# Kernel tuning notes

Hardware: AMD Instinct MI355X
Metric: run time of the kernel (lower is better)

Reference implementation:

```python
import jax, jax.numpy as jnp
import numpy as np

N = 8192        # num nodes (bs in the original docstring)
D_IN = 512      # input feature dim
HEADS = 8
DPH = 512 // HEADS  # size_per_head = hidden_size // num_heads
EDGE_P = 0.01   # adjacency density


def setup_inputs() -> dict:
    key = jax.random.key(0)
    k1, k2, k3 = jax.random.split(key, 3)
    H = jax.random.normal(k1, (N, D_IN), dtype=jnp.float32)
    # dense 0/1 adjacency, as passed to the layer before tf.sparse.from_dense
    adj = (jax.random.uniform(k2, (N, N)) < EDGE_P).astype(jnp.float32)
    # Glorot-uniform per-head projection kernels, stacked: (HEADS, D_IN, DPH)
    limit = float(np.sqrt(6.0 / (D_IN + DPH)))
    W = jax.random.uniform(k3, (HEADS, D_IN, DPH), jnp.float32, -limit, limit)
    b = jnp.zeros((HEADS, DPH), jnp.float32)
    return {"H": H, "adj": adj, "W": W, "b": b}


def reference(H, adj, W, b):
    # Per-head dense projection: H_ = H @ W_h  -> (HEADS, N, DPH)
    H_ = jnp.einsum('nd,hde->hne', H, W)
    # NOTE: the original layer computes a sparse sigmoid/softmax attention
    # (f1 + f2^T over adj) but never uses it: head_output uses raw adj.
    # Aggregation: adj @ H_ per head, plus bias; activation = tf.identity.
    out = jnp.einsum('nm,hme->hne', adj, H_) + b[:, None, :]  # (HEADS, N, DPH)
    # Concat heads along feature axis (head 0 first) -> (N, HEADS*DPH)
    return jnp.transpose(out, (1, 0, 2)).reshape(H.shape[0], HEADS * DPH)
```

## Files before the change

### kernel.cpp

```cpp
#include <hip/hip_runtime.h>
#include <hip/hip_bf16.h>

typedef __attribute__((ext_vector_type(8))) short short8;
typedef __attribute__((ext_vector_type(4))) float floatx4;

#define GN 8192
#define GD 512
#define MAXDEG 256
#define GEMM_BLOCKS 512

static __device__ __forceinline__ ushort bf16bits(float x) {
  __hip_bfloat16 h = __float2bfloat16(x);
  return *(ushort*)&h;
}
static __device__ __forceinline__ float bf16f(uint u16) {
  return __uint_as_float(u16 << 16);
}

__global__ void detect_kernel(const uint* __restrict__ H, const uint* __restrict__ W,
                              const uint* __restrict__ adj, const uint* __restrict__ b,
                              int* __restrict__ flags, float* __restrict__ bias) {
  __shared__ int cH, cW, cA, cB;
  const int t = threadIdx.x;
  if (t == 0) { cH = 0; cW = 0; cA = 0; cB = 0; }
  __syncthreads();
  { const uint e = (H[t] >> 7) & 0xFFu; if (e >= 100u && e <= 140u) atomicAdd(&cH, 1); }
  { const uint e = (W[t] >> 7) & 0xFFu; if (e >= 100u && e <= 140u) atomicAdd(&cW, 1); }
  for (int i = t; i < 4096; i += 256)
    if ((adj[i] & 0xFFFFu) == 0x3F80u) atomicAdd(&cA, 1);
  if (b[t] != 0u) atomicAdd(&cB, 1);
  __syncthreads();
  const int hb = cH > 128, wb = cW > 128, ab = cA > 0;
  if (t == 0) { flags[0] = hb; flags[1] = wb; flags[2] = ab; }
  if (cB == 0) {
    bias[t] = 0.0f; bias[t + 256] = 0.0f;
  } else if (wb) {
    const ushort* bs = (const ushort*)b;
    bias[t] = bf16f(bs[t]); bias[t + 256] = bf16f(bs[t + 256]);
  } else {
    const float* bf = (const float*)b;
    bias[t] = bf[t]; bias[t + 256] = bf[t + 256];
  }
}

#define BM 128
#define BN 64
#define BK 64
#define LDK 72

#define SMEM_BYTES (BM * LDK * 2 + BN * LDK * 2)

__global__ __launch_bounds__(256) void fused_kernel(
    const void* __restrict__ Hv, const void* __restrict__ Wv,
    const void* __restrict__ adjv, ushort* __restrict__ HP,
    int* __restrict__ rowcnt, uint2* __restrict__ edges,
    const int* __restrict__ flags) {
  __shared__ __align__(16) unsigned char smem[SMEM_BYTES];

  const int tid = threadIdx.x;

  if (blockIdx.x < GEMM_BLOCKS) {
    ushort* sA = (ushort*)smem;
    ushort* sB = (ushort*)(smem + BM * LDK * 2);
    const int hb = flags[0];
    const int wb = flags[1];
    const int bn = blockIdx.x & 7;
    const int bm = blockIdx.x >> 3;
    const int m0 = bm * BM;
    const int lane = tid & 63;
    const int w = tid >> 6;
    const int wr = w >> 1, wc = w & 1;
    const int l15 = lane & 15, q = lane >> 4;

    floatx4 acc[4][2];
#pragma unroll
    for (int i = 0; i < 4; i++)
#pragma unroll
      for (int j = 0; j < 2; j++) acc[i][j] = (floatx4)0.0f;

    for (int k0 = 0; k0 < GD; k0 += BK) {
      __syncthreads();
      if (hb) {
        const ushort* H16 = (const ushort*)Hv;
        const int r = tid >> 3;
        const int kc = (tid & 7) * 8;
#pragma unroll
        for (int p = 0; p < 4; p++) {
          const int row = r + p * 32;
          const uint4 v = *(const uint4*)(H16 + (size_t)(m0 + row) * GD + k0 + kc);
          *(uint4*)(sA + row * LDK + kc) = v;
        }
      } else {
        const float* H32 = (const float*)Hv;
        const int r0 = tid >> 4;
        const int kc = (tid & 15) * 4;
#pragma unroll
        for (int p = 0; p < 8; p++) {
          const int row = r0 + p * 16;
          const float4 v = *(const float4*)(H32 + (size_t)(m0 + row) * GD + k0 + kc);
          ushort4 o;
          o.x = bf16bits(v.x); o.y = bf16bits(v.y);
          o.z = bf16bits(v.z); o.w = bf16bits(v.w);
          *(ushort4*)(sA + row * LDK + kc) = o;
        }
      }
      if (wb) {
        const ushort* Wh = (const ushort*)Wv + (size_t)bn * (512 * 64);
        const int kk = tid >> 3;
        const int e0 = (tid & 7) * 8;
#pragma unroll
        for (int p = 0; p < 2; p++) {
          const int k = kk + p * 32;
          const uint4 v = *(const uint4*)(Wh + (size_t)(k0 + k) * 64 + e0);
          const ushort* pv = (const ushort*)&v;
#pragma unroll
          for (int j = 0; j < 8; j++) sB[(e0 + j) * LDK + k] = pv[j];
        }
      } else {
        const float* Wh = (const float*)Wv + (size_t)bn * (512 * 64);
        const int kk = tid >> 4;
        const int e0 = (tid & 15) * 4;
#pragma unroll
        for (int p = 0; p < 4; p++) {
          const int k = kk + p * 16;
          const float4 v = *(const float4*)(Wh + (size_t)(k0 + k) * 64 + e0);
          sB[(e0 + 0) * LDK + k] = bf16bits(v.x);
          sB[(e0 + 1) * LDK + k] = bf16bits(v.y);
          sB[(e0 + 2) * LDK + k] = bf16bits(v.z);
          sB[(e0 + 3) * LDK + k] = bf16bits(v.w);
        }
      }
      __syncthreads();
#pragma unroll
      for (int kq = 0; kq < 2; kq++) {
        short8 af[4], bfv[2];
#pragma unroll
        for (int mt = 0; mt < 4; mt++)
          af[mt] = *(const short8*)(sA + (wr * 64 + mt * 16 + l15) * LDK + kq * 32 + q * 8);
#pragma unroll
        for (int ct = 0; ct < 2; ct++)
          bfv[ct] = *(const short8*)(sB + (wc * 32 + ct * 16 + l15) * LDK + kq * 32 + q * 8);
#pragma unroll
        for (int mt = 0; mt < 4; mt++)
#pragma unroll
          for (int ct = 0; ct < 2; ct++)
            acc[mt][ct] = __builtin_amdgcn_mfma_f32_16x16x32_bf16(
                af[mt], bfv[ct], acc[mt][ct], 0, 0, 0);
      }
    }
#pragma unroll
    for (int mt = 0; mt < 4; mt++)
#pragma unroll
      for (int ct = 0; ct < 2; ct++)
#pragma unroll
        for (int r = 0; r < 4; r++) {
          const int row = m0 + wr * 64 + mt * 16 + q * 4 + r;
          const int col = bn * 64 + wc * 32 + ct * 16 + l15;
          HP[(size_t)row * GD + col] = bf16bits(acc[mt][ct][r]);
        }
  } else {
    int* s_idx = (int*)smem;
    float* s_val = (float*)(smem + 1024);
    int* s_cnt = (int*)(smem + 2048);
    const int ab = flags[2];
    const int n = blockIdx.x - GEMM_BLOCKS;
    const int t = tid;
    if (t == 0) *s_cnt = 0;
    __syncthreads();
    if (ab) {
      const ushort* arow = (const ushort*)adjv + (size_t)n * GN;
#pragma unroll
      for (int c = 0; c < 8; c++) {
        const int c0 = c * 1024;
        const uint2 v = *(const uint2*)(arow + c0 + t * 4);
        const uint e[4] = {v.x & 0xFFFFu, v.x >> 16, v.y & 0xFFFFu, v.y >> 16};
#pragma unroll
        for (int j = 0; j < 4; j++)
          if (e[j] != 0u) {
            const int pos = atomicAdd(s_cnt, 1);
            if (pos < MAXDEG) { s_idx[pos] = c0 + t * 4 + j; s_val[pos] = bf16f(e[j]); }
          }
      }
    } else {
      const float* arow = (const float*)adjv + (size_t)n * GN;
#pragma unroll
      for (int c = 0; c < 8; c++) {
        const int c0 = c * 1024;
        const float4 v = *(const float4*)(arow + c0 + t * 4);
        const float pv[4] = {v.x, v.y, v.z, v.w};
#pragma unroll
        for (int j = 0; j < 4; j++)
          if (pv[j] != 0.0f) {
            const int pos = atomicAdd(s_cnt, 1);
            if (pos < MAXDEG) { s_idx[pos] = c0 + t * 4 + j; s_val[pos] = pv[j]; }
          }
      }
    }
    __syncthreads();
    const int cnt = min(*s_cnt, MAXDEG);
    if (t == 0) rowcnt[n] = cnt;
    if (t < cnt) {
      uint2 e; e.x = (uint)s_idx[t]; e.y = __float_as_uint(s_val[t]);
      edges[(size_t)n * MAXDEG + t] = e;
    }
  }
}

__global__ __launch_bounds__(128) void gather_kernel(
    const ushort* __restrict__ HP, const int* __restrict__ rowcnt,
    const uint2* __restrict__ edges, const float* __restrict__ bias,
    float* __restrict__ out) {
  __shared__ int s_idx[MAXDEG];
  __shared__ float s_val[MAXDEG];

  const int b = blockIdx.x;
  const int half = b & 1;
  const int n = b >> 1;
  const int t = threadIdx.x;
  const int cnt = rowcnt[n];

  for (int i = t; i < cnt; i += 128) {
    const uint2 e = edges[(size_t)n * MAXDEG + i];
    s_idx[i] = (int)e.x;
    s_val[i] = __uint_as_float(e.y);
  }
  __syncthreads();

  const uint* HPu = (const uint*)HP;
  const int co = (half << 7) + t;
  float acc0 = 0.0f, acc1 = 0.0f;
  int i = 0;
  for (; i + 4 <= cnt; i += 4) {
    const int m0_ = s_idx[i + 0], m1_ = s_idx[i + 1];
    const int m2_ = s_idx[i + 2], m3_ = s_idx[i + 3];
    const float v0 = s_val[i + 0], v1 = s_val[i + 1];
    const float v2 = s_val[i + 2], v3 = s_val[i + 3];
    const uint u0 = HPu[(size_t)m0_ * 256 + co];
    const uint u1 = HPu[(size_t)m1_ * 256 + co];
    const uint u2 = HPu[(size_t)m2_ * 256 + co];
    const uint u3 = HPu[(size_t)m3_ * 256 + co];
    acc0 += v0 * bf16f(u0 & 0xFFFFu) + v1 * bf16f(u1 & 0xFFFFu);
    acc0 += v2 * bf16f(u2 & 0xFFFFu) + v3 * bf16f(u3 & 0xFFFFu);
    acc1 += v0 * __uint_as_float(u0 & 0xFFFF0000u) + v1 * __uint_as_float(u1 & 0xFFFF0000u);
    acc1 += v2 * __uint_as_float(u2 & 0xFFFF0000u) + v3 * __uint_as_float(u3 & 0xFFFF0000u);
  }
  for (; i < cnt; i++) {
    const int m_ = s_idx[i];
    const float vv = s_val[i];
    const uint u = HPu[(size_t)m_ * 256 + co];
    acc0 += vv * bf16f(u & 0xFFFFu);
    acc1 += vv * __uint_as_float(u & 0xFFFF0000u);
  }

  const float2 bb = ((const float2*)bias)[co];
  float2 o;
  o.x = acc0 + bb.x;
  o.y = acc1 + bb.y;
  ((float2*)out)[(size_t)n * 256 + co] = o;
}

extern "C" void kernel_launch(void* const* d_in, const int* in_sizes, int n_in,
                              void* d_out, int out_size, void* d_ws, size_t ws_size,
                              hipStream_t stream) {
  const void *H = d_in[0], *adj = d_in[1], *W = d_in[2], *b = d_in[3];
  for (int i = 0; i < n_in; i++) {
    const int s = in_sizes[i];
    if (s == GN * GN) adj = d_in[i];
    else if (s == GN * GD) H = d_in[i];
    else if (s == 8 * 512 * 64) W = d_in[i];
    else if (s == 512) b = d_in[i];
  }
  float* out = (float*)d_out;

  char* ws = (char*)d_ws;
  ushort* HP   = (ushort*)ws;
  float*  bias = (float*)(ws + (size_t)GN * GD * 2);
  int*    flags= (int*)(ws + (size_t)GN * GD * 2 + 2048);
  int*  rowcnt = (int*)(ws + (size_t)GN * GD * 2 + 4096);
  uint2* edges = (uint2*)(ws + (size_t)GN * GD * 2 + 4096 + GN * 4);

  detect_kernel<<<1, 256, 0, stream>>>((const uint*)H, (const uint*)W,
                                       (const uint*)adj, (const uint*)b,
                                       flags, bias);
  fused_kernel<<<GEMM_BLOCKS + GN, 256, 0, stream>>>(H, W, adj, HP,
                                                     rowcnt, edges, flags);
  gather_kernel<<<GN * 2, 128, 0, stream>>>(HP, rowcnt, edges, bias, out);
}
```

Measured before the change: 432.5 us.

## Replace sparse edge-list gather with dense split-K MFMA GEMM over adjacency

After: 504.3 us. 16.6% more time.

```diff
diff --git a/kernel.cpp b/kernel.cpp
--- a/kernel.cpp
+++ b/kernel.cpp
@@ -3,10 +3,10 @@
 
 typedef __attribute__((ext_vector_type(8))) short short8;
 typedef __attribute__((ext_vector_type(4))) float floatx4;
+typedef __attribute__((ext_vector_type(4))) uint uintx4;
 
 #define GN 8192
 #define GD 512
-#define MAXDEG 256
 #define GEMM_BLOCKS 512
 
 static __device__ __forceinline__ ushort bf16bits(float x) {
@@ -15,6 +15,12 @@
 }
 static __device__ __forceinline__ float bf16f(uint u16) {
   return __uint_as_float(u16 << 16);
+}
+
+typedef __attribute__((address_space(1))) const void g1_void;
+typedef __attribute__((address_space(3))) void l3_void;
+static __device__ __forceinline__ void gl_lds16(const void* g, void* l) {
+  __builtin_amdgcn_global_load_lds((g1_void*)g, (l3_void*)l, 16, 0, 0);
 }
 
 __global__ void detect_kernel(const uint* __restrict__ H, const uint* __restrict__ W,
@@ -50,213 +56,216 @@
 
 #define SMEM_BYTES (BM * LDK * 2 + BN * LDK * 2)
 
-__global__ __launch_bounds__(256) void fused_kernel(
+__global__ __launch_bounds__(256) void proj_kernel(
     const void* __restrict__ Hv, const void* __restrict__ Wv,
-    const void* __restrict__ adjv, ushort* __restrict__ HP,
-    int* __restrict__ rowcnt, uint2* __restrict__ edges,
-    const int* __restrict__ flags) {
+    ushort* __restrict__ HPt, const int* __restrict__ flags) {
   __shared__ __align__(16) unsigned char smem[SMEM_BYTES];
-
+  ushort* sA = (ushort*)smem;
+  ushort* sB = (ushort*)(smem + BM * LDK * 2);
   const int tid = threadIdx.x;
-
-  if (blockIdx.x < GEMM_BLOCKS) {
-    ushort* sA = (ushort*)smem;
-    ushort* sB = (ushort*)(smem + BM * LDK * 2);
-    const int hb = flags[0];
-    const int wb = flags[1];
-    const int bn = blockIdx.x & 7;
-    const int bm = blockIdx.x >> 3;
-    const int m0 = bm * BM;
-    const int lane = tid & 63;
-    const int w = tid >> 6;
-    const int wr = w >> 1, wc = w & 1;
-    const int l15 = lane & 15, q = lane >> 4;
-
-    floatx4 acc[4][2];
-#pragma unroll
-    for (int i = 0; i < 4; i++)
-#pragma unroll
-      for (int j = 0; j < 2; j++) acc[i][j] = (floatx4)0.0f;
-
-    for (int k0 = 0; k0 < GD; k0 += BK) {
-      __syncthreads();
-      if (hb) {
-        const ushort* H16 = (const ushort*)Hv;
-        const int r = tid >> 3;
-        const int kc = (tid & 7) * 8;
-#pragma unroll
-        for (int p = 0; p < 4; p++) {
-          const int row = r + p * 32;
-          const uint4 v = *(const uint4*)(H16 + (size_t)(m0 + row) * GD + k0 + kc);
-          *(uint4*)(sA + row * LDK + kc) = v;
-        }
-      } else {
-        const float* H32 = (const float*)Hv;
-        const int r0 = tid >> 4;
-        const int kc = (tid & 15) * 4;
-#pragma unroll
-        for (int p = 0; p < 8; p++) {
-          const int row = r0 + p * 16;
-          const float4 v = *(const float4*)(H32 + (size_t)(m0 + row) * GD + k0 + kc);
-          ushort4 o;
-          o.x = bf16bits(v.x); o.y = bf16bits(v.y);
-          o.z = bf16bits(v.z); o.w = bf16bits(v.w);
-          *(ushort4*)(sA + row * LDK + kc) = o;
-        }
-      }
-      if (wb) {
-        const ushort* Wh = (const ushort*)Wv + (size_t)bn * (512 * 64);
-        const int kk = tid >> 3;
-        const int e0 = (tid & 7) * 8;
-#pragma unroll
-        for (int p = 0; p < 2; p++) {
-          const int k = kk + p * 32;
-          const uint4 v = *(const uint4*)(Wh + (size_t)(k0 + k) * 64 + e0);
-          const ushort* pv = (const ushort*)&v;
-#pragma unroll
-          for (int j = 0; j < 8; j++) sB[(e0 + j) * LDK + k] = pv[j];
-        }
-      } else {
-        const float* Wh = (const float*)Wv + (size_t)bn * (512 * 64);
-        const int kk = tid >> 4;
-        const int e0 = (tid & 15) * 4;
-#pragma unroll
-        for (int p = 0; p < 4; p++) {
-          const int k = kk + p * 16;
-          const float4 v = *(const float4*)(Wh + (size_t)(k0 + k) * 64 + e0);
-          sB[(e0 + 0) * LDK + k] = bf16bits(v.x);
-          sB[(e0 + 1) * LDK + k] = bf16bits(v.y);
-          sB[(e0 + 2) * LDK + k] = bf16bits(v.z);
-          sB[(e0 + 3) * LDK + k] = bf16bits(v.w);
-        }
-      }
-      __syncthreads();
-#pragma unroll
-      for (int kq = 0; kq < 2; kq++) {
-        short8 af[4], bfv[2];
-#pragma unroll
-        for (int mt = 0; mt < 4; mt++)
-          af[mt] = *(const short8*)(sA + (wr * 64 + mt * 16 + l15) * LDK + kq * 32 + q * 8);
+  const int hb = flags[0];
+  const int wb = flags[1];
+  const int bn = blockIdx.x & 7;
+  const int bm = blockIdx.x >> 3;
+  const int m0 = bm * BM;
+  const int lane = tid & 63;
+  const int w = tid >> 6;
+  const int wr = w >> 1, wc = w & 1;
+  const int l15 = lane & 15, q = lane >> 4;
+
+  floatx4 acc[4][2];
+#pragma unroll
+  for (int i = 0; i < 4; i++)
+#pragma unroll
+    for (int j = 0; j < 2; j++) acc[i][j] = (floatx4)0.0f;
+
+  for (int k0 = 0; k0 < GD; k0 += BK) {
+    __syncthreads();
+    if (hb) {
+      const ushort* H16 = (const ushort*)Hv;
+      const int r = tid >> 3;
+      const int kc = (tid & 7) * 8;
+#pragma unroll
+      for (int p = 0; p < 4; p++) {
+        const int row = r + p * 32;
+        const uint4 v = *(const uint4*)(H16 + (size_t)(m0 + row) * GD + k0 + kc);
+        *(uint4*)(sA + row * LDK + kc) = v;
+      }
+    } else {
+      const float* H32 = (const float*)Hv;
+      const int r0 = tid >> 4;
+      const int kc = (tid & 15) * 4;
+#pragma unroll
+      for (int p = 0; p < 8; p++) {
+        const int row = r0 + p * 16;
+        const float4 v = *(const float4*)(H32 + (size_t)(m0 + row) * GD + k0 + kc);
+        ushort4 o;
+        o.x = bf16bits(v.x); o.y = bf16bits(v.y);
+        o.z = bf16bits(v.z); o.w = bf16bits(v.w);
+        *(ushort4*)(sA + row * LDK + kc) = o;
+      }
+    }
+    if (wb) {
+      const ushort* Wh = (const ushort*)Wv + (size_t)bn * (512 * 64);
+      const int kk = tid >> 3;
+      const int e0 = (tid & 7) * 8;
+#pragma unroll
+      for (int p = 0; p < 2; p++) {
+        const int k = kk + p * 32;
+        const uint4 v = *(const uint4*)(Wh + (size_t)(k0 + k) * 64 + e0);
+        const ushort* pv = (const ushort*)&v;
+#pragma unroll
+        for (int j = 0; j < 8; j++) sB[(e0 + j) * LDK + k] = pv[j];
+      }
+    } else {
+      const float* Wh = (const float*)Wv + (size_t)bn * (512 * 64);
+      const int kk = tid >> 4;
+      const int e0 = (tid & 15) * 4;
+#pragma unroll
+      for (int p = 0; p < 4; p++) {
+        const int k = kk + p * 16;
+        const float4 v = *(const float4*)(Wh + (size_t)(k0 + k) * 64 + e0);
+        sB[(e0 + 0) * LDK + k] = bf16bits(v.x);
+        sB[(e0 + 1) * LDK + k] = bf16bits(v.y);
+        sB[(e0 + 2) * LDK + k] = bf16bits(v.z);
+        sB[(e0 + 3) * LDK + k] = bf16bits(v.w);
+      }
+    }
+    __syncthreads();
+#pragma unroll
+    for (int kq = 0; kq < 2; kq++) {
+      short8 af[4], bfv[2];
+#pragma unroll
+      for (int mt = 0; mt < 4; mt++)
+        af[mt] = *(const short8*)(sA + (wr * 64 + mt * 16 + l15) * LDK + kq * 32 + q * 8);
+#pragma unroll
+      for (int ct = 0; ct < 2; ct++)
+        bfv[ct] = *(const short8*)(sB + (wc * 32 + ct * 16 + l15) * LDK + kq * 32 + q * 8);
+#pragma unroll
+      for (int mt = 0; mt < 4; mt++)
 #pragma unroll
         for (int ct = 0; ct < 2; ct++)
-          bfv[ct] = *(const short8*)(sB + (wc * 32 + ct * 16 + l15) * LDK + kq * 32 + q * 8);
-#pragma unroll
-        for (int mt = 0; mt < 4; mt++)
-#pragma unroll
-          for (int ct = 0; ct < 2; ct++)
-            acc[mt][ct] = __builtin_amdgcn_mfma_f32_16x16x32_bf16(
-                af[mt], bfv[ct], acc[mt][ct], 0, 0, 0);
-      }
-    }
-#pragma unroll
-    for (int mt = 0; mt < 4; mt++)
-#pragma unroll
-      for (int ct = 0; ct < 2; ct++)
-#pragma unroll
-        for (int r = 0; r < 4; r++) {
-          const int row = m0 + wr * 64 + mt * 16 + q * 4 + r;
-          const int col = bn * 64 + wc * 32 + ct * 16 + l15;
-          HP[(size_t)row * GD + col] = bf16bits(acc[mt][ct][r]);
-        }
-  } else {
-    int* s_idx = (int*)smem;
-    float* s_val = (float*)(smem + 1024);
-    int* s_cnt = (int*)(smem + 2048);
-    const int ab = flags[2];
-    const int n = blockIdx.x - GEMM_BLOCKS;
-    const int t = tid;
-    if (t == 0) *s_cnt = 0;
-    __syncthreads();
+          acc[mt][ct] = __builtin_amdgcn_mfma_f32_16x16x32_bf16(
+              af[mt], bfv[ct], acc[mt][ct], 0, 0, 0);
+    }
+  }
+#pragma unroll
+  for (int mt = 0; mt < 4; mt++)
+#pragma unroll
+    for (int ct = 0; ct < 2; ct++) {
+      const int col = bn * 64 + wc * 32 + ct * 16 + l15;
+      const int rowb = m0 + wr * 64 + mt * 16 + q * 4;
+      ushort4 o;
+      o.x = bf16bits(acc[mt][ct][0]);
+      o.y = bf16bits(acc[mt][ct][1]);
+      o.z = bf16bits(acc[mt][ct][2]);
+      o.w = bf16bits(acc[mt][ct][3]);
+      *(ushort4*)(HPt + (size_t)col * GN + rowb) = o;
+    }
+}
+
+#define ABM 64
+#define ABK 64
+#define AKCH 4096
+#define ALDA 72
+
+__global__ __launch_bounds__(512) void agg_kernel(
+    const void* __restrict__ adjv, const ushort* __restrict__ HPt,
+    float* __restrict__ pbuf, const int* __restrict__ flags) {
+  __shared__ __align__(16) ushort sA[ABM * ALDA];
+  __shared__ __align__(16) ushort sB[GD * 64];
+  const int ab = flags[2];
+  const int bid = blockIdx.x;
+  const int kch = bid & 1;
+  const int m0 = (bid >> 1) * ABM;
+  const size_t kb = (size_t)kch * AKCH;
+  const int tid = threadIdx.x;
+  const int lane = tid & 63, w = tid >> 6;
+  const int l15 = lane & 15, q = lane >> 4;
+
+  floatx4 acc[4][4];
+#pragma unroll
+  for (int i = 0; i < 4; i++)
+#pragma unroll
+    for (int j = 0; j < 4; j++) acc[i][j] = (floatx4)0.0f;
+
+  const int be0 = w * 8 + (lane >> 3);
+  const int bkc = (lane & 7) * 8;
+
+  for (int k0 = 0; k0 < AKCH; k0 += ABK) {
+    __syncthreads();
+#pragma unroll
+    for (int p = 0; p < 8; p++) {
+      const int e = p * 64 + be0;
+      gl_lds16(HPt + (size_t)e * GN + kb + k0 + bkc,
+               sB + (size_t)(p * 64 + w * 8) * 64);
+    }
     if (ab) {
-      const ushort* arow = (const ushort*)adjv + (size_t)n * GN;
-#pragma unroll
-      for (int c = 0; c < 8; c++) {
-        const int c0 = c * 1024;
-        const uint2 v = *(const uint2*)(arow + c0 + t * 4);
-        const uint e[4] = {v.x & 0xFFFFu, v.x >> 16, v.y & 0xFFFFu, v.y >> 16};
-#pragma unroll
-        for (int j = 0; j < 4; j++)
-          if (e[j] != 0u) {
-            const int pos = atomicAdd(s_cnt, 1);
-            if (pos < MAXDEG) { s_idx[pos] = c0 + t * 4 + j; s_val[pos] = bf16f(e[j]); }
-          }
-      }
+      const ushort* adj16 = (const ushort*)adjv;
+      const int n = tid >> 3;
+      const int kc = (tid & 7) * 8;
+      const uintx4 v = __builtin_nontemporal_load(
+          (const uintx4*)(adj16 + (size_t)(m0 + n) * GN + kb + k0 + kc));
+      *(uintx4*)(sA + n * ALDA + kc) = v;
     } else {
-      const float* arow = (const float*)adjv + (size_t)n * GN;
-#pragma unroll
-      for (int c = 0; c < 8; c++) {
-        const int c0 = c * 1024;
-        const float4 v = *(const float4*)(arow + c0 + t * 4);
-        const float pv[4] = {v.x, v.y, v.z, v.w};
-#pragma unroll
-        for (int j = 0; j < 4; j++)
-          if (pv[j] != 0.0f) {
-            const int pos = atomicAdd(s_cnt, 1);
-            if (pos < MAXDEG) { s_idx[pos] = c0 + t * 4 + j; s_val[pos] = pv[j]; }
-          }
-      }
-    }
-    __syncthreads();
-    const int cnt = min(*s_cnt, MAXDEG);
-    if (t == 0) rowcnt[n] = cnt;
-    if (t < cnt) {
-      uint2 e; e.x = (uint)s_idx[t]; e.y = __float_as_uint(s_val[t]);
-      edges[(size_t)n * MAXDEG + t] = e;
-    }
-  }
-}
-
-__global__ __launch_bounds__(128) void gather_kernel(
-    const ushort* __restrict__ HP, const int* __restrict__ rowcnt,
-    const uint2* __restrict__ edges, const float* __restrict__ bias,
-    float* __restrict__ out) {
-  __shared__ int s_idx[MAXDEG];
-  __shared__ float s_val[MAXDEG];
-
-  const int b = blockIdx.x;
-  const int half = b & 1;
-  const int n = b >> 1;
-  const int t = threadIdx.x;
-  const int cnt = rowcnt[n];
-
-  for (int i = t; i < cnt; i += 128) {
-    const uint2 e = edges[(size_t)n * MAXDEG + i];
-    s_idx[i] = (int)e.x;
-    s_val[i] = __uint_as_float(e.y);
-  }
-  __syncthreads();
-
-  const uint* HPu = (const uint*)HP;
-  const int co = (half << 7) + t;
-  float acc0 = 0.0f, acc1 = 0.0f;
-  int i = 0;
-  for (; i + 4 <= cnt; i += 4) {
-    const int m0_ = s_idx[i + 0], m1_ = s_idx[i + 1];
-    const int m2_ = s_idx[i + 2], m3_ = s_idx[i + 3];
-    const float v0 = s_val[i + 0], v1 = s_val[i + 1];
-    const float v2 = s_val[i + 2], v3 = s_val[i + 3];
-    const uint u0 = HPu[(size_t)m0_ * 256 + co];
-    const uint u1 = HPu[(size_t)m1_ * 256 + co];
-    const uint u2 = HPu[(size_t)m2_ * 256 + co];
-    const uint u3 = HPu[(size_t)m3_ * 256 + co];
-    acc0 += v0 * bf16f(u0 & 0xFFFFu) + v1 * bf16f(u1 & 0xFFFFu);
-    acc0 += v2 * bf16f(u2 & 0xFFFFu) + v3 * bf16f(u3 & 0xFFFFu);
-    acc1 += v0 * __uint_as_float(u0 & 0xFFFF0000u) + v1 * __uint_as_float(u1 & 0xFFFF0000u);
-    acc1 += v2 * __uint_as_float(u2 & 0xFFFF0000u) + v3 * __uint_as_float(u3 & 0xFFFF0000u);
-  }
-  for (; i < cnt; i++) {
-    const int m_ = s_idx[i];
-    const float vv = s_val[i];
-    const uint u = HPu[(size_t)m_ * 256 + co];
-    acc0 += vv * bf16f(u & 0xFFFFu);
-    acc1 += vv * __uint_as_float(u & 0xFFFF0000u);
-  }
-
-  const float2 bb = ((const float2*)bias)[co];
-  float2 o;
-  o.x = acc0 + bb.x;
-  o.y = acc1 + bb.y;
-  ((float2*)out)[(size_t)n * 256 + co] = o;
+      const float* adj32 = (const float*)adjv;
+      const int n = tid >> 3;
+      const int kc = (tid & 7) * 8;
+      const float* src = adj32 + (size_t)(m0 + n) * GN + kb + k0 + kc;
+      const floatx4 v0 = __builtin_nontemporal_load((const floatx4*)src);
+      const floatx4 v1 = __builtin_nontemporal_load((const floatx4*)(src + 4));
+      ushort4 o0, o1;
+      o0.x = bf16bits(v0.x); o0.y = bf16bits(v0.y);
+      o0.z = bf16bits(v0.z); o0.w = bf16bits(v0.w);
+      o1.x = bf16bits(v1.x); o1.y = bf16bits(v1.y);
+      o1.z = bf16bits(v1.z); o1.w = bf16bits(v1.w);
+      *(ushort4*)(sA + n * ALDA + kc) = o0;
+      *(ushort4*)(sA + n * ALDA + kc + 4) = o1;
+    }
+    __syncthreads();
+#pragma unroll
+    for (int kq = 0; kq < 2; kq++) {
+      short8 af[4], bfr[4];
+#pragma unroll
+      for (int mt = 0; mt < 4; mt++)
+        af[mt] = *(const short8*)(sA + (mt * 16 + l15) * ALDA + kq * 32 + q * 8);
+#pragma unroll
+      for (int ct = 0; ct < 4; ct++)
+        bfr[ct] = *(const short8*)(sB + (w * 64 + ct * 16 + l15) * 64 + kq * 32 + q * 8);
+#pragma unroll
+      for (int mt = 0; mt < 4; mt++)
+#pragma unroll
+        for (int ct = 0; ct < 4; ct++)
+          acc[mt][ct] = __builtin_amdgcn_mfma_f32_16x16x32_bf16(
+              af[mt], bfr[ct], acc[mt][ct], 0, 0, 0);
+    }
+  }
+  float* pb = pbuf + (size_t)kch * ((size_t)GN * GD);
+#pragma unroll
+  for (int mt = 0; mt < 4; mt++)
+#pragma unroll
+    for (int ct = 0; ct < 4; ct++) {
+      const int col = w * 64 + ct * 16 + l15;
+      const int rowb = m0 + mt * 16 + q * 4;
+#pragma unroll
+      for (int r = 0; r < 4; r++)
+        pb[(size_t)(rowb + r) * GD + col] = acc[mt][ct][r];
+    }
+}
+
+__global__ __launch_bounds__(256) void combine_kernel(
+    const float* __restrict__ p0, const float* __restrict__ p1,
+    const float* __restrict__ bias, float* __restrict__ out) {
+  const int i = blockIdx.x * 256 + threadIdx.x;
+  const floatx4 a = __builtin_nontemporal_load((const floatx4*)p0 + i);
+  const floatx4 b = __builtin_nontemporal_load((const floatx4*)p1 + i);
+  const floatx4 bb = *((const floatx4*)bias + (i & 127));
+  floatx4 o;
+  o.x = a.x + b.x + bb.x;
+  o.y = a.y + b.y + bb.y;
+  o.z = a.z + b.z + bb.z;
+  o.w = a.w + b.w + bb.w;
+  __builtin_nontemporal_store(o, (floatx4*)out + i);
 }
 
 extern "C" void kernel_launch(void* const* d_in, const int* in_sizes, int n_in,
@@ -273,16 +282,15 @@
   float* out = (float*)d_out;
 
   char* ws = (char*)d_ws;
-  ushort* HP   = (ushort*)ws;
+  ushort* HPt  = (ushort*)ws;
   float*  bias = (float*)(ws + (size_t)GN * GD * 2);
-  int*    flags= (int*)(ws + (size_t)GN * GD * 2 + 2048);
-  int*  rowcnt = (int*)(ws + (size_t)GN * GD * 2 + 4096);
-  uint2* edges = (uint2*)(ws + (size_t)GN * GD * 2 + 4096 + GN * 4);
+  int*    flags= (int*)(ws + (size_t)GN * GD * 2 + 4096);
+  float*  pbuf = (float*)(ws + (size_t)16 * 1024 * 1024);
 
   detect_kernel<<<1, 256, 0, stream>>>((const uint*)H, (const uint*)W,
                                        (const uint*)adj, (const uint*)b,
                                        flags, bias);
-  fused_kernel<<<GEMM_BLOCKS + GN, 256, 0, stream>>>(H, W, adj, HP,
-                                                     rowcnt, edges, flags);
-  gather_kernel<<<GN * 2, 128, 0, stream>>>(HP, rowcnt, edges, bias, out);
-}
+  proj_kernel<<<GEMM_BLOCKS, 256, 0, stream>>>(H, W, HPt, flags);
+  agg_kernel<<<256, 512, 0, stream>>>(adj, HPt, pbuf, flags);
+  combine_kernel<<<4096, 256, 0, stream>>>(pbuf, pbuf + (size_t)GN * GD, bias, out);
+}
```
